# Performance work log

Hardware: AMD Instinct MI355X
Metric: run time of the kernel (lower is better)

## Reference

```python
import jax, jax.numpy as jnp
import numpy as np

N, E, G = 100000, 1600000, 500
F_IN, H, OUT, MD = 128, 128, 1, 30


def gcn_conv(x, src, dst, ew, W, b):
    # PyG GCNConv: x' = D^-1/2 (A + I) D^-1/2 (x W) + b, with edge weights ew
    n = x.shape[0]
    h = x @ W  # [N, H]
    loops = jnp.arange(n)
    s = jnp.concatenate([src, loops])
    d = jnp.concatenate([dst, loops])
    w = jnp.concatenate([ew, jnp.ones((n,), dtype=x.dtype)])
    deg = jax.ops.segment_sum(w, d, num_segments=n)
    dinv = jnp.where(deg > 0, jax.lax.rsqrt(deg), 0.0).astype(x.dtype)
    norm = dinv[s] * w * dinv[d]  # [E+N]
    out = jax.ops.segment_sum(norm[:, None] * h[s], d, num_segments=n)
    return out + b


def setup_inputs() -> dict:
    key = jax.random.key(0)
    ks = jax.random.split(key, 12)
    x = jax.random.normal(ks[0], (N, F_IN), dtype=jnp.float32)
    edge_index = jax.random.randint(ks[1], (2, E), 0, N, dtype=jnp.int64)
    edge_attr = jax.random.uniform(ks[2], (E,), dtype=jnp.float32)
    batch = jnp.sort(jax.random.randint(ks[3], (N,), 0, G, dtype=jnp.int64))
    metadata = jax.random.normal(ks[4], (G, MD), dtype=jnp.float32)
    s = lambda fi, fo: 1.0 / np.sqrt(fi)
    W1 = jax.random.normal(ks[5], (F_IN, H), dtype=jnp.float32) * s(F_IN, H)
    b1 = jnp.zeros((H,), dtype=jnp.float32)
    W2 = jax.random.normal(ks[6], (H, H), dtype=jnp.float32) * s(H, H)
    b2 = jnp.zeros((H,), dtype=jnp.float32)
    Wm = jax.random.normal(ks[7], (MD, H), dtype=jnp.float32) * s(MD, H)
    bm = jnp.zeros((H,), dtype=jnp.float32)
    Wf = jax.random.normal(ks[8], (2 * H, OUT), dtype=jnp.float32) * s(2 * H, OUT)
    bf = jnp.zeros((OUT,), dtype=jnp.float32)
    return {"x": x, "edge_index": edge_index, "edge_attr": edge_attr,
            "batch": batch, "metadata": metadata,
            "W1": W1, "b1": b1, "W2": W2, "b2": b2,
            "Wm": Wm, "bm": bm, "Wf": Wf, "bf": bf}


def reference(x, edge_index, edge_attr, batch, metadata, W1, b1, W2, b2, Wm, bm, Wf, bf):
    src, dst = edge_index[0], edge_index[1]
    h = jax.nn.relu(gcn_conv(x, src, dst, edge_attr, W1, b1))
    h = jax.nn.relu(gcn_conv(h, src, dst, edge_attr, W2, b2))
    # global_mean_pool over batch ids
    sums = jax.ops.segment_sum(h, batch, num_segments=G)
    cnt = jax.ops.segment_sum(jnp.ones((h.shape[0],), h.dtype), batch, num_segments=G)
    pooled = sums / jnp.maximum(cnt, 1.0)[:, None]  # [G, H]
    # per-graph metadata: first node index of graph i, idx = first_node % M
    first_node = jax.ops.segment_min(jnp.arange(batch.shape[0]), batch, num_segments=G)
    idx = first_node % metadata.shape[0]
    md = metadata[idx]  # [G, MD]
    md = jax.nn.relu(md @ Wm + bm)  # dropout inactive at eval
    z = jnp.concatenate([pooled, md], axis=1)
    return z @ Wf + bf
```

## Files before the change

kernel.cpp:

```cpp
#include <hip/hip_runtime.h>
#include <cstdint>


#define BK_SHIFT 9
#define BK_NODES 512
#define CH 4096
#define NODE_BITS 17
#define NODE_MASK ((1 << NODE_BITS) - 1)

typedef short bf16x8 __attribute__((ext_vector_type(8)));
typedef float f32x4 __attribute__((ext_vector_type(4)));

union bfpack {
    uint4 u;
    bf16x8 b;
};

static __device__ __forceinline__ unsigned int f2bf(float f) {
    unsigned int u = __float_as_uint(f);
    return (u + 0x7fffu + ((u >> 16) & 1u)) >> 16;
}
static __device__ __forceinline__ unsigned int packbf2(float a, float b) {
    return f2bf(a) | (f2bf(b) << 16);
}
static __device__ __forceinline__ float bf_lo(unsigned int v) {
    return __uint_as_float(v << 16);
}
static __device__ __forceinline__ float bf_hi(unsigned int v) {
    return __uint_as_float(v & 0xffff0000u);
}

__global__ void k_init_small(int* gstart, int* gend, int G, int* bcnt, int NBK) {
    int g = blockIdx.x * blockDim.x + threadIdx.x;
    if (g < G) { gstart[g] = 0x7fffffff; gend[g] = 0; }
    if (g < NBK) bcnt[g] = 0;
}

__global__ void k_init_nodes(const int* __restrict__ batch,
                             int* __restrict__ gstart, int* __restrict__ gend, int N) {
    int i = blockIdx.x * blockDim.x + threadIdx.x;
    if (i >= N) return;
    int b = batch[i];
    if (i == 0 || batch[i - 1] != b) gstart[b] = i;
    if (i == N - 1 || batch[i + 1] != b) gend[b] = i + 1;
}

__global__ __launch_bounds__(256) void k_binhist(const int* __restrict__ dst, int E,
                                                 int* __restrict__ bcnt, int NBK) {
    __shared__ int h[256];
    int tid = threadIdx.x;
    h[tid] = 0;
    __syncthreads();
    int base = blockIdx.x * CH;
    int nend = min(base + CH, E);
    for (int i = base + tid; i < nend; i += 256) atomicAdd(&h[dst[i] >> BK_SHIFT], 1);
    __syncthreads();
    if (tid < NBK && h[tid]) atomicAdd(&bcnt[tid], h[tid]);
}

__global__ __launch_bounds__(256) void k_binscan(const int* __restrict__ bcnt,
                                                 int* __restrict__ bbase,
                                                 int* __restrict__ bfill, int NBK) {
    __shared__ int sc[256];
    int tid = threadIdx.x;
    int v = (tid < NBK) ? bcnt[tid] : 0;
    sc[tid] = v;
    __syncthreads();
    for (int d = 1; d < 256; d <<= 1) {
        int t = (tid >= d) ? sc[tid - d] : 0;
        __syncthreads();
        sc[tid] += t;
        __syncthreads();
    }
    int excl = sc[tid] - v;
    if (tid < NBK) { bbase[tid] = excl; bfill[tid] = excl; }
    if (tid == 255) bbase[NBK] = sc[255];
}

__global__ __launch_bounds__(256) void k_binscatter(const int* __restrict__ src,
                                                    const int* __restrict__ dst,
                                                    const float* __restrict__ ew,
                                                    int* __restrict__ bfill,
                                                    int2* __restrict__ binned, int E) {
    __shared__ int2 stage2[CH];
    __shared__ unsigned char bkt2[CH];
    __shared__ int hist[256], sc[256], lofs[256], cnt2[256], gbase[256];
    int tid = threadIdx.x;
    int base = blockIdx.x * CH;
    int n = min(CH, E - base);
    hist[tid] = 0;
    cnt2[tid] = 0;
    __syncthreads();
    int2 ev[CH / 256];
    int bk[CH / 256];
#pragma unroll
    for (int j = 0; j < CH / 256; ++j) {
        int i = base + tid + j * 256;
        bk[j] = -1;
        if (i < base + n) {
            int s = src[i], d = dst[i];
            float w = ew[i];
            int b = d >> BK_SHIFT;
            ev[j] = make_int2(s | ((d & (BK_NODES - 1)) << NODE_BITS), __float_as_int(w));
            bk[j] = b;
            atomicAdd(&hist[b], 1);
        }
    }
    __syncthreads();
    int hv = hist[tid];
    sc[tid] = hv;
    __syncthreads();
    for (int d = 1; d < 256; d <<= 1) {
        int t = (tid >= d) ? sc[tid - d] : 0;
        __syncthreads();
        sc[tid] += t;
        __syncthreads();
    }
    lofs[tid] = sc[tid] - hv;
    gbase[tid] = hv ? atomicAdd(&bfill[tid], hv) : 0;
    __syncthreads();
#pragma unroll
    for (int j = 0; j < CH / 256; ++j) {
        if (bk[j] >= 0) {
            int r = atomicAdd(&cnt2[bk[j]], 1);
            int p = lofs[bk[j]] + r;
            stage2[p] = ev[j];
            bkt2[p] = (unsigned char)bk[j];
        }
    }
    __syncthreads();
    for (int i = tid; i < n; i += 256) {
        int b = bkt2[i];
        binned[gbase[b] + (i - lofs[b])] = stage2[i];
    }
}

__global__ __launch_bounds__(256) void k_csr(const int2* __restrict__ binned,
                                             const int* __restrict__ bbase,
                                             int2* __restrict__ cvb,
                                             int* __restrict__ rowptr,
                                             float* __restrict__ dinv, int N, int E) {
    __shared__ int lh[BK_NODES];
    __shared__ float ls[BK_NODES];
    __shared__ int lofs[BK_NODES];
    __shared__ int s2[256];
    int tid = threadIdx.x;
    int b = blockIdx.x;
    int nbase = b << BK_SHIFT;
    int nend = min(nbase + BK_NODES, N);
    int ebase = bbase[b], eend = bbase[b + 1];
    for (int i = tid; i < BK_NODES; i += 256) { lh[i] = 0; ls[i] = 0.f; }
    __syncthreads();
    for (int e = ebase + tid; e < eend; e += 256) {
        int2 v = binned[e];
        int local = (v.x >> NODE_BITS) & (BK_NODES - 1);
        atomicAdd(&lh[local], 1);
        atomicAdd(&ls[local], __int_as_float(v.y));
    }
    __syncthreads();
    int p0 = lh[2 * tid], p1 = lh[2 * tid + 1];
    int pv = p0 + p1;
    s2[tid] = pv;
    __syncthreads();
    for (int d = 1; d < 256; d <<= 1) {
        int t = (tid >= d) ? s2[tid - d] : 0;
        __syncthreads();
        s2[tid] += t;
        __syncthreads();
    }
    int e2 = s2[tid] - pv;
    lofs[2 * tid] = e2;
    lofs[2 * tid + 1] = e2 + p0;
    __syncthreads();
    for (int i = nbase + tid; i < nend; i += 256) {
        int local = i - nbase;
        rowptr[i] = ebase + lofs[local];
        dinv[i] = rsqrtf(1.0f + ls[local]);
    }
    if (b == 0 && tid == 0) rowptr[N] = E;
    __syncthreads();
    for (int e = ebase + tid; e < eend; e += 256) {
        int2 v = binned[e];
        int local = (v.x >> NODE_BITS) & (BK_NODES - 1);
        int r = atomicAdd(&lofs[local], 1);
        cvb[ebase + r] = make_int2(v.x & NODE_MASK, v.y);
    }
}

__global__ __launch_bounds__(256) void k_wt(const float* __restrict__ W,
                                            unsigned short* __restrict__ WT) {
    int idx = blockIdx.x * 256 + threadIdx.x;
    int n = idx >> 7, k = idx & 127;
    WT[idx] = (unsigned short)f2bf(W[(size_t)k * 128 + n]);
}

__global__ __launch_bounds__(256) void k_gemm1(const float* __restrict__ X,
                                               const unsigned short* __restrict__ WT,
                                               const float* __restrict__ dinv,
                                               unsigned short* __restrict__ Y, int M) {
    int tid = threadIdx.x;
    int wid = tid >> 6, lane = tid & 63;
    int rowb = blockIdx.x * 64 + wid * 16;
    int r16 = lane & 15, kg = lane >> 4;
    int arow = min(rowb + r16, M - 1);
    const float* xr = X + (size_t)arow * 128 + kg * 8;
    bf16x8 a[4];
#pragma unroll
    for (int kc = 0; kc < 4; ++kc) {
        float4 u = *reinterpret_cast<const float4*>(xr + kc * 32);
        float4 v = *reinterpret_cast<const float4*>(xr + kc * 32 + 4);
        bfpack pk;
        pk.u = make_uint4(packbf2(u.x, u.y), packbf2(u.z, u.w),
                          packbf2(v.x, v.y), packbf2(v.z, v.w));
        a[kc] = pk.b;
    }
    float dv[4];
#pragma unroll
    for (int r = 0; r < 4; ++r) {
        int ro = rowb + kg * 4 + r;
        dv[r] = (ro < M) ? dinv[ro] : 0.f;
    }
    const bf16x8* Bp = reinterpret_cast<const bf16x8*>(WT + (size_t)r16 * 128 + kg * 8);
#pragma unroll
    for (int nt = 0; nt < 8; ++nt) {
        const bf16x8* B = Bp + (size_t)nt * 256;
        f32x4 acc = {0.f, 0.f, 0.f, 0.f};
        acc = __builtin_amdgcn_mfma_f32_16x16x32_bf16(a[0], B[0], acc, 0, 0, 0);
        acc = __builtin_amdgcn_mfma_f32_16x16x32_bf16(a[1], B[4], acc, 0, 0, 0);
        acc = __builtin_amdgcn_mfma_f32_16x16x32_bf16(a[2], B[8], acc, 0, 0, 0);
        acc = __builtin_amdgcn_mfma_f32_16x16x32_bf16(a[3], B[12], acc, 0, 0, 0);
        int colo = nt * 16 + r16;
#pragma unroll
        for (int r = 0; r < 4; ++r) {
            int ro = rowb + kg * 4 + r;
            if (ro < M) Y[(size_t)ro * 128 + colo] = (unsigned short)f2bf(acc[r] * dv[r]);
        }
    }
}

__global__ __launch_bounds__(256) void k_gemm(const unsigned short* __restrict__ Xb,
                                              const unsigned short* __restrict__ WT,
                                              const float* __restrict__ dinv,
                                              unsigned short* __restrict__ Y, int M) {
    int tid = threadIdx.x;
    int wid = tid >> 6, lane = tid & 63;
    int rowb = blockIdx.x * 64 + wid * 16;
    int r16 = lane & 15, kg = lane >> 4;
    const bf16x8* Ap = reinterpret_cast<const bf16x8*>(Xb + (size_t)(rowb + r16) * 128 + kg * 8);
    bf16x8 a0 = Ap[0], a1 = Ap[4], a2 = Ap[8], a3 = Ap[12];
    float dv[4];
#pragma unroll
    for (int r = 0; r < 4; ++r) {
        int ro = rowb + kg * 4 + r;
        dv[r] = (ro < M) ? dinv[ro] : 0.f;
    }
    const bf16x8* Bp = reinterpret_cast<const bf16x8*>(WT + (size_t)r16 * 128 + kg * 8);
#pragma unroll
    for (int nt = 0; nt < 8; ++nt) {
        const bf16x8* B = Bp + (size_t)nt * 256;
        f32x4 acc = {0.f, 0.f, 0.f, 0.f};
        acc = __builtin_amdgcn_mfma_f32_16x16x32_bf16(a0, B[0], acc, 0, 0, 0);
        acc = __builtin_amdgcn_mfma_f32_16x16x32_bf16(a1, B[4], acc, 0, 0, 0);
        acc = __builtin_amdgcn_mfma_f32_16x16x32_bf16(a2, B[8], acc, 0, 0, 0);
        acc = __builtin_amdgcn_mfma_f32_16x16x32_bf16(a3, B[12], acc, 0, 0, 0);
        int colo = nt * 16 + r16;
#pragma unroll
        for (int r = 0; r < 4; ++r) {
            int ro = rowb + kg * 4 + r;
            if (ro < M) Y[(size_t)ro * 128 + colo] = (unsigned short)f2bf(acc[r] * dv[r]);
        }
    }
}

__global__ __launch_bounds__(256) void k_agg(const uint2* __restrict__ Hb2,
                                             const int* __restrict__ rowptr,
                                             const int2* __restrict__ cvb,
                                             const float* __restrict__ dinv,
                                             const float* __restrict__ bias,
                                             uint2* __restrict__ OutB2, int N) {
    __shared__ int2 lcv[4][4][2][64];
    int tid = threadIdx.x;
    int lane = tid & 63, wid = tid >> 6;
    int half = lane >> 5, sl = lane & 31;
    int n0 = (blockIdx.x * 4 + wid) * 8;
    if (n0 >= N) return;
    int rv = rowptr[min(n0 + min(lane, 8), N)];
    int rp[9];
#pragma unroll
    for (int k = 0; k < 9; ++k) rp[k] = __shfl(rv, k);
    int cnt[8];
    int nmax = 0;
#pragma unroll
    for (int k = 0; k < 8; ++k) {
        cnt[k] = rp[k + 1] - rp[k];
        nmax = max(nmax, cnt[k]);
    }
    float a[4][4];
#pragma unroll
    for (int s = 0; s < 4; ++s) {
        int ns = n0 + 2 * s + half;
        uint2 hv = (ns < N) ? Hb2[(size_t)ns * 32 + sl] : make_uint2(0u, 0u);
        a[s][0] = bf_lo(hv.x);
        a[s][1] = bf_hi(hv.x);
        a[s][2] = bf_lo(hv.y);
        a[s][3] = bf_hi(hv.y);
    }
    for (int base = 0; base < nmax; base += 64) {
#pragma unroll
        for (int s = 0; s < 4; ++s) {
#pragma unroll
            for (int h = 0; h < 2; ++h) {
                int k = 2 * s + h;
                int2 t = (base + lane < cnt[k]) ? cvb[rp[k] + base + lane]
                                                : make_int2(0, 0);
                lcv[wid][s][h][lane] = t;
            }
        }
        int m = min(64, nmax - base);
        for (int j0 = 0; j0 < m; j0 += 8) {
#pragma unroll
            for (int jj = 0; jj < 8; ++jj) {
                int j = j0 + jj;
                if (j < m) {
                    int2 e0 = lcv[wid][0][half][j];
                    int2 e1 = lcv[wid][1][half][j];
                    int2 e2 = lcv[wid][2][half][j];
                    int2 e3 = lcv[wid][3][half][j];
                    uint2 h0 = Hb2[(size_t)e0.x * 32 + sl];
                    uint2 h1 = Hb2[(size_t)e1.x * 32 + sl];
                    uint2 h2 = Hb2[(size_t)e2.x * 32 + sl];
                    uint2 h3 = Hb2[(size_t)e3.x * 32 + sl];
                    float w0 = __int_as_float(e0.y);
                    float w1 = __int_as_float(e1.y);
                    float w2 = __int_as_float(e2.y);
                    float w3 = __int_as_float(e3.y);
                    a[0][0] = fmaf(w0, bf_lo(h0.x), a[0][0]);
                    a[0][1] = fmaf(w0, bf_hi(h0.x), a[0][1]);
                    a[0][2] = fmaf(w0, bf_lo(h0.y), a[0][2]);
                    a[0][3] = fmaf(w0, bf_hi(h0.y), a[0][3]);
                    a[1][0] = fmaf(w1, bf_lo(h1.x), a[1][0]);
                    a[1][1] = fmaf(w1, bf_hi(h1.x), a[1][1]);
                    a[1][2] = fmaf(w1, bf_lo(h1.y), a[1][2]);
                    a[1][3] = fmaf(w1, bf_hi(h1.y), a[1][3]);
                    a[2][0] = fmaf(w2, bf_lo(h2.x), a[2][0]);
                    a[2][1] = fmaf(w2, bf_hi(h2.x), a[2][1]);
                    a[2][2] = fmaf(w2, bf_lo(h2.y), a[2][2]);
                    a[2][3] = fmaf(w2, bf_hi(h2.y), a[2][3]);
                    a[3][0] = fmaf(w3, bf_lo(h3.x), a[3][0]);
                    a[3][1] = fmaf(w3, bf_hi(h3.x), a[3][1]);
                    a[3][2] = fmaf(w3, bf_lo(h3.y), a[3][2]);
                    a[3][3] = fmaf(w3, bf_hi(h3.y), a[3][3]);
                }
            }
        }
    }
    float4 bv = reinterpret_cast<const float4*>(bias)[sl];
#pragma unroll
    for (int s = 0; s < 4; ++s) {
        int ns = n0 + 2 * s + half;
        if (ns < N) {
            float d = dinv[ns];
            float o0 = fmaxf(fmaf(a[s][0], d, bv.x), 0.f);
            float o1 = fmaxf(fmaf(a[s][1], d, bv.y), 0.f);
            float o2 = fmaxf(fmaf(a[s][2], d, bv.z), 0.f);
            float o3 = fmaxf(fmaf(a[s][3], d, bv.w), 0.f);
            OutB2[(size_t)ns * 32 + sl] = make_uint2(packbf2(o0, o1), packbf2(o2, o3));
        }
    }
}

__global__ __launch_bounds__(256) void k_poolhead(const unsigned int* __restrict__ H2u,
                                                  const int* __restrict__ gstart,
                                                  const int* __restrict__ gend,
                                                  const float* __restrict__ meta,
                                                  const float* __restrict__ Wm,
                                                  const float* __restrict__ bm,
                                                  const float* __restrict__ Wf,
                                                  const float* __restrict__ bf,
                                                  float* __restrict__ out, int G) {
    int g = blockIdx.x;
    int tid = threadIdx.x;
    int cu = tid & 63, q = tid >> 6;
    __shared__ float r0[256], r1[256];
    __shared__ float pooled[128];
    __shared__ float red[128];
    int b = gstart[g];
    int e = gend[g];
    int cntg = e - b;
    float s0 = 0.f, s1 = 0.f;
    for (int i = q; i < cntg; i += 4) {
        unsigned int v = H2u[(size_t)(b + i) * 64 + cu];
        s0 += bf_lo(v);
        s1 += bf_hi(v);
    }
    r0[tid] = s0; r1[tid] = s1;
    __syncthreads();
    if (tid < 64) {
        float t0 = r0[cu] + r0[cu + 64] + r0[cu + 128] + r0[cu + 192];
        float t1 = r1[cu] + r1[cu + 64] + r1[cu + 128] + r1[cu + 192];
        float inv = 1.f / fmaxf((float)cntg, 1.f);
        pooled[2 * cu] = t0 * inv;
        pooled[2 * cu + 1] = t1 * inv;
    }
    __syncthreads();
    if (tid < 128) {
        int c = tid;
        int idx = gstart[g] % G;
        float m = bm[c];
#pragma unroll
        for (int k = 0; k < 30; ++k) m = fmaf(meta[idx * 30 + k], Wm[k * 128 + c], m);
        m = fmaxf(m, 0.f);
        red[c] = pooled[c] * Wf[c] + m * Wf[128 + c];
    }
    __syncthreads();
    for (int st = 64; st > 0; st >>= 1) {
        if (tid < st) red[tid] += red[tid + st];
        __syncthreads();
    }
    if (tid == 0) out[g] = red[0] + bf[0];
}

extern "C" void kernel_launch(void* const* d_in, const int* in_sizes, int n_in,
                              void* d_out, int out_size, void* d_ws, size_t ws_size,
                              hipStream_t stream) {
    const float* x     = (const float*)d_in[0];
    const int*   ei    = (const int*)d_in[1];
    const float* ew    = (const float*)d_in[2];
    const int*   batch = (const int*)d_in[3];
    const float* meta  = (const float*)d_in[4];
    const float* W1    = (const float*)d_in[5];
    const float* b1    = (const float*)d_in[6];
    const float* W2    = (const float*)d_in[7];
    const float* b2    = (const float*)d_in[8];
    const float* Wm    = (const float*)d_in[9];
    const float* bm    = (const float*)d_in[10];
    const float* Wf    = (const float*)d_in[11];
    const float* bf    = (const float*)d_in[12];

    int N = in_sizes[0] / 128;
    int E = in_sizes[2];
    int G = in_sizes[4] / 30;
    int Mpad = (N + 63) & ~63;
    int NBK = (N + BK_NODES - 1) >> BK_SHIFT;
    const int* srcp = ei;
    const int* dstp = ei + E;

    char* p = (char*)d_ws;
    auto alloc = [&](size_t bytes) -> void* {
        void* r = p;
        p += (bytes + 255) & ~(size_t)255;
        return r;
    };
    float* dinv   = (float*)alloc((size_t)N * 4);
    int*   rowptr = (int*)alloc((size_t)(N + 1) * 4);
    int2*  binned = (int2*)alloc((size_t)E * 8);
    int2*  cvb    = (int2*)alloc((size_t)E * 8);
    int*   bcnt   = (int*)alloc((size_t)NBK * 4);
    int*   bbase  = (int*)alloc((size_t)(NBK + 1) * 4);
    int*   bfillp = (int*)alloc((size_t)NBK * 4);
    unsigned short* H   = (unsigned short*)alloc((size_t)Mpad * 128 * 2);
    unsigned short* H2  = (unsigned short*)alloc((size_t)Mpad * 128 * 2);
    unsigned short* WT1 = (unsigned short*)alloc(128 * 128 * 2);
    unsigned short* WT2 = (unsigned short*)alloc(128 * 128 * 2);
    int*   gstart = (int*)alloc((size_t)G * 4);
    int*   gend   = (int*)alloc((size_t)G * 4);

    int EB = (E + CH - 1) / CH;
    k_init_small<<<(max(G, NBK) + 255) / 256, 256, 0, stream>>>(gstart, gend, G, bcnt, NBK);
    k_init_nodes<<<(N + 255) / 256, 256, 0, stream>>>(batch, gstart, gend, N);
    k_binhist<<<EB, 256, 0, stream>>>(dstp, E, bcnt, NBK);
    k_binscan<<<1, 256, 0, stream>>>(bcnt, bbase, bfillp, NBK);
    k_binscatter<<<EB, 256, 0, stream>>>(srcp, dstp, ew, bfillp, binned, E);
    k_csr<<<NBK, 256, 0, stream>>>(binned, bbase, cvb, rowptr, dinv, N, E);

    k_wt<<<64, 256, 0, stream>>>(W1, WT1);
    k_wt<<<64, 256, 0, stream>>>(W2, WT2);

    k_gemm1<<<Mpad / 64, 256, 0, stream>>>(x, WT1, dinv, H, N);
    k_agg<<<(N + 31) / 32, 256, 0, stream>>>((const uint2*)H, rowptr, cvb, dinv, b1,
                                             (uint2*)H2, N);
    k_gemm<<<Mpad / 64, 256, 0, stream>>>(H2, WT2, dinv, H, N);
    k_agg<<<(N + 31) / 32, 256, 0, stream>>>((const uint2*)H, rowptr, cvb, dinv, b2,
                                             (uint2*)H2, N);

    k_poolhead<<<G, 256, 0, stream>>>((const unsigned int*)H2, gstart, gend,
                                      meta, Wm, bm, Wf, bf, (float*)d_out, G);
}
```

Before: 299.1 us.

## Fuse layer-1 aggregation with layer-2 GEMM and merge weight transposes

Layer-1 aggregation is fused with the layer-2 GEMM. Each 32-node block writes its relu'd bf16 rows into shared memory, and the block's four waves then run the MFMA GEMM against WT2 directly. This removes one full write and read of the N×128 intermediate and one kernel launch. The two weight-transpose kernels are also merged into one launch. The trade-off is an extra __syncthreads and shared memory per aggregation block, which may lower occupancy in the gather-bound kernel.

```diff
diff --git a/kernel.cpp b/kernel.cpp
--- a/kernel.cpp
+++ b/kernel.cpp
@@ -187,11 +187,16 @@
     }
 }
 
-__global__ __launch_bounds__(256) void k_wt(const float* __restrict__ W,
-                                            unsigned short* __restrict__ WT) {
+__global__ __launch_bounds__(256) void k_wtboth(const float* __restrict__ W1,
+                                                const float* __restrict__ W2,
+                                                unsigned short* __restrict__ WT1,
+                                                unsigned short* __restrict__ WT2) {
     int idx = blockIdx.x * 256 + threadIdx.x;
-    int n = idx >> 7, k = idx & 127;
-    WT[idx] = (unsigned short)f2bf(W[(size_t)k * 128 + n]);
+    const float* W = (idx < 16384) ? W1 : W2;
+    unsigned short* WT = (idx < 16384) ? WT1 : WT2;
+    int i = idx & 16383;
+    int n = i >> 7, k = i & 127;
+    WT[i] = (unsigned short)f2bf(W[(size_t)k * 128 + n]);
 }
 
 __global__ __launch_bounds__(256) void k_gemm1(const float* __restrict__ X,
@@ -238,36 +243,146 @@
     }
 }
 
-__global__ __launch_bounds__(256) void k_gemm(const unsigned short* __restrict__ Xb,
-                                              const unsigned short* __restrict__ WT,
-                                              const float* __restrict__ dinv,
-                                              unsigned short* __restrict__ Y, int M) {
-    int tid = threadIdx.x;
-    int wid = tid >> 6, lane = tid & 63;
-    int rowb = blockIdx.x * 64 + wid * 16;
+__global__ __launch_bounds__(256) void k_aggemm(const uint2* __restrict__ Hb2,
+                                                const int* __restrict__ rowptr,
+                                                const int2* __restrict__ cvb,
+                                                const float* __restrict__ dinv,
+                                                const float* __restrict__ bias,
+                                                const unsigned short* __restrict__ WT2,
+                                                unsigned short* __restrict__ Y, int N) {
+    __shared__ int2 lcv[4][4][2][64];
+    __shared__ uint2 hst[32][33];
+    int tid = threadIdx.x;
+    int lane = tid & 63, wid = tid >> 6;
+    int half = lane >> 5, sl = lane & 31;
+    int blockbase = blockIdx.x * 32;
+    int n0 = blockbase + wid * 8;
+    bool active = (n0 < N);
+    float a[4][4];
+#pragma unroll
+    for (int s = 0; s < 4; ++s)
+#pragma unroll
+        for (int q = 0; q < 4; ++q) a[s][q] = 0.f;
+    if (active) {
+        int rv = rowptr[min(n0 + min(lane, 8), N)];
+        int rp[9];
+#pragma unroll
+        for (int k = 0; k < 9; ++k) rp[k] = __shfl(rv, k);
+        int cnt[8];
+        int nmax = 0;
+#pragma unroll
+        for (int k = 0; k < 8; ++k) {
+            cnt[k] = rp[k + 1] - rp[k];
+            nmax = max(nmax, cnt[k]);
+        }
+#pragma unroll
+        for (int s = 0; s < 4; ++s) {
+            int ns = n0 + 2 * s + half;
+            uint2 hv = (ns < N) ? Hb2[(size_t)ns * 32 + sl] : make_uint2(0u, 0u);
+            a[s][0] = bf_lo(hv.x);
+            a[s][1] = bf_hi(hv.x);
+            a[s][2] = bf_lo(hv.y);
+            a[s][3] = bf_hi(hv.y);
+        }
+        for (int base = 0; base < nmax; base += 64) {
+#pragma unroll
+            for (int s = 0; s < 4; ++s) {
+#pragma unroll
+                for (int h = 0; h < 2; ++h) {
+                    int k = 2 * s + h;
+                    int2 t = (base + lane < cnt[k]) ? cvb[rp[k] + base + lane]
+                                                    : make_int2(0, 0);
+                    lcv[wid][s][h][lane] = t;
+                }
+            }
+            int m = min(64, nmax - base);
+            for (int j0 = 0; j0 < m; j0 += 8) {
+#pragma unroll
+                for (int jj = 0; jj < 8; ++jj) {
+                    int j = j0 + jj;
+                    if (j < m) {
+                        int2 e0 = lcv[wid][0][half][j];
+                        int2 e1 = lcv[wid][1][half][j];
+                        int2 e2 = lcv[wid][2][half][j];
+                        int2 e3 = lcv[wid][3][half][j];
+                        uint2 h0 = Hb2[(size_t)e0.x * 32 + sl];
+                        uint2 h1 = Hb2[(size_t)e1.x * 32 + sl];
+                        uint2 h2 = Hb2[(size_t)e2.x * 32 + sl];
+                        uint2 h3 = Hb2[(size_t)e3.x * 32 + sl];
+                        float w0 = __int_as_float(e0.y);
+                        float w1 = __int_as_float(e1.y);
+                        float w2 = __int_as_float(e2.y);
+                        float w3 = __int_as_float(e3.y);
+                        a[0][0] = fmaf(w0, bf_lo(h0.x), a[0][0]);
+                        a[0][1] = fmaf(w0, bf_hi(h0.x), a[0][1]);
+                        a[0][2] = fmaf(w0, bf_lo(h0.y), a[0][2]);
+                        a[0][3] = fmaf(w0, bf_hi(h0.y), a[0][3]);
+                        a[1][0] = fmaf(w1, bf_lo(h1.x), a[1][0]);
+                        a[1][1] = fmaf(w1, bf_hi(h1.x), a[1][1]);
+                        a[1][2] = fmaf(w1, bf_lo(h1.y), a[1][2]);
+                        a[1][3] = fmaf(w1, bf_hi(h1.y), a[1][3]);
+                        a[2][0] = fmaf(w2, bf_lo(h2.x), a[2][0]);
+                        a[2][1] = fmaf(w2, bf_hi(h2.x), a[2][1]);
+                        a[2][2] = fmaf(w2, bf_lo(h2.y), a[2][2]);
+                        a[2][3] = fmaf(w2, bf_hi(h2.y), a[2][3]);
+                        a[3][0] = fmaf(w3, bf_lo(h3.x), a[3][0]);
+                        a[3][1] = fmaf(w3, bf_hi(h3.x), a[3][1]);
+                        a[3][2] = fmaf(w3, bf_lo(h3.y), a[3][2]);
+                        a[3][3] = fmaf(w3, bf_hi(h3.y), a[3][3]);
+                    }
+                }
+            }
+        }
+    }
+    float4 bv = reinterpret_cast<const float4*>(bias)[sl];
+#pragma unroll
+    for (int s = 0; s < 4; ++s) {
+        int ns = n0 + 2 * s + half;
+        uint2 o = make_uint2(0u, 0u);
+        if (active && ns < N) {
+            float d = dinv[ns];
+            float o0 = fmaxf(fmaf(a[s][0], d, bv.x), 0.f);
+            float o1 = fmaxf(fmaf(a[s][1], d, bv.y), 0.f);
+            float o2 = fmaxf(fmaf(a[s][2], d, bv.z), 0.f);
+            float o3 = fmaxf(fmaf(a[s][3], d, bv.w), 0.f);
+            o = make_uint2(packbf2(o0, o1), packbf2(o2, o3));
+        }
+        hst[wid * 8 + 2 * s + half][sl] = o;
+    }
+    __syncthreads();
     int r16 = lane & 15, kg = lane >> 4;
-    const bf16x8* Ap = reinterpret_cast<const bf16x8*>(Xb + (size_t)(rowb + r16) * 128 + kg * 8);
-    bf16x8 a0 = Ap[0], a1 = Ap[4], a2 = Ap[8], a3 = Ap[12];
+    int trow = wid >> 1;
+    int ntb = (wid & 1) * 4;
+    int arow = trow * 16 + r16;
+    bf16x8 afr[4];
+#pragma unroll
+    for (int kc = 0; kc < 4; ++kc) {
+        uint2 lo = hst[arow][kc * 8 + kg * 2];
+        uint2 hi = hst[arow][kc * 8 + kg * 2 + 1];
+        bfpack pk;
+        pk.u = make_uint4(lo.x, lo.y, hi.x, hi.y);
+        afr[kc] = pk.b;
+    }
     float dv[4];
 #pragma unroll
     for (int r = 0; r < 4; ++r) {
-        int ro = rowb + kg * 4 + r;
-        dv[r] = (ro < M) ? dinv[ro] : 0.f;
-    }
-    const bf16x8* Bp = reinterpret_cast<const bf16x8*>(WT + (size_t)r16 * 128 + kg * 8);
-#pragma unroll
-    for (int nt = 0; nt < 8; ++nt) {
-        const bf16x8* B = Bp + (size_t)nt * 256;
+        int ro = blockbase + trow * 16 + kg * 4 + r;
+        dv[r] = (ro < N) ? dinv[ro] : 0.f;
+    }
+    const bf16x8* Bp = reinterpret_cast<const bf16x8*>(WT2 + (size_t)r16 * 128 + kg * 8);
+#pragma unroll
+    for (int nt = 0; nt < 4; ++nt) {
+        const bf16x8* B = Bp + (size_t)(ntb + nt) * 256;
         f32x4 acc = {0.f, 0.f, 0.f, 0.f};
-        acc = __builtin_amdgcn_mfma_f32_16x16x32_bf16(a0, B[0], acc, 0, 0, 0);
-        acc = __builtin_amdgcn_mfma_f32_16x16x32_bf16(a1, B[4], acc, 0, 0, 0);
-        acc = __builtin_amdgcn_mfma_f32_16x16x32_bf16(a2, B[8], acc, 0, 0, 0);
-        acc = __builtin_amdgcn_mfma_f32_16x16x32_bf16(a3, B[12], acc, 0, 0, 0);
-        int colo = nt * 16 + r16;
+        acc = __builtin_amdgcn_mfma_f32_16x16x32_bf16(afr[0], B[0], acc, 0, 0, 0);
+        acc = __builtin_amdgcn_mfma_f32_16x16x32_bf16(afr[1], B[4], acc, 0, 0, 0);
+        acc = __builtin_amdgcn_mfma_f32_16x16x32_bf16(afr[2], B[8], acc, 0, 0, 0);
+        acc = __builtin_amdgcn_mfma_f32_16x16x32_bf16(afr[3], B[12], acc, 0, 0, 0);
+        int colo = (ntb + nt) * 16 + r16;
 #pragma unroll
         for (int r = 0; r < 4; ++r) {
-            int ro = rowb + kg * 4 + r;
-            if (ro < M) Y[(size_t)ro * 128 + colo] = (unsigned short)f2bf(acc[r] * dv[r]);
+            int ro = blockbase + trow * 16 + kg * 4 + r;
+            if (ro < N) Y[(size_t)ro * 128 + colo] = (unsigned short)f2bf(acc[r] * dv[r]);
         }
     }
 }
@@ -473,16 +588,15 @@
     k_binscatter<<<EB, 256, 0, stream>>>(srcp, dstp, ew, bfillp, binned, E);
     k_csr<<<NBK, 256, 0, stream>>>(binned, bbase, cvb, rowptr, dinv, N, E);
 
-    k_wt<<<64, 256, 0, stream>>>(W1, WT1);
-    k_wt<<<64, 256, 0, stream>>>(W2, WT2);
+    k_wtboth<<<128, 256, 0, stream>>>(W1, W2, WT1, WT2);
 
     k_gemm1<<<Mpad / 64, 256, 0, stream>>>(x, WT1, dinv, H, N);
-    k_agg<<<(N + 31) / 32, 256, 0, stream>>>((const uint2*)H, rowptr, cvb, dinv, b1,
-                                             (uint2*)H2, N);
-    k_gemm<<<Mpad / 64, 256, 0, stream>>>(H2, WT2, dinv, H, N);
-    k_agg<<<(N + 31) / 32, 256, 0, stream>>>((const uint2*)H, rowptr, cvb, dinv, b2,
-                                             (uint2*)H2, N);
-
-    k_poolhead<<<G, 256, 0, stream>>>((const unsigned int*)H2, gstart, gend,
+    int NB32 = (N + 31) / 32;
+    k_aggemm<<<NB32, 256, 0, stream>>>((const uint2*)H, rowptr, cvb, dinv, b1, WT2,
+                                       H2, N);
+    k_agg<<<NB32, 256, 0, stream>>>((const uint2*)H2, rowptr, cvb, dinv, b2,
+                                    (uint2*)H, N);
+
+    k_poolhead<<<G, 256, 0, stream>>>((const unsigned int*)H, gstart, gend,
                                       meta, Wm, bm, Wf, bf, (float*)d_out, G);
 }
```

Result: faster. 290.9 us (-2.8%).
